# Kernel tuning notes

Measured on AMD Instinct MI355X. Metric: run time of the kernel, lower is better.

The kernel has to match this reference:

```python
import jax, jax.numpy as jnp
import numpy as np

N = 100000
E = 1600000
IN_DIM = 64
EMB_DIM = 64
BN_EPS = 1e-5


def setup_inputs() -> dict:
    key = jax.random.key(0)
    ks = jax.random.split(key, 8)
    x = jax.random.normal(ks[0], (N, IN_DIM), dtype=jnp.float32)
    edge_index = jax.random.randint(ks[1], (2, E), 0, N, dtype=jnp.int64)
    # GIN learned epsilon (train_eps=True), initialized to 0 as in PyG
    eps = jnp.zeros((), dtype=jnp.float32)
    # MLP params: Linear(in, emb) -> BN -> ReLU -> Linear(emb, emb)
    s1 = 1.0 / np.sqrt(IN_DIM)
    W1 = jax.random.uniform(ks[2], (IN_DIM, EMB_DIM), jnp.float32, -s1, s1)
    b1 = jax.random.uniform(ks[3], (EMB_DIM,), jnp.float32, -s1, s1)
    gamma = jnp.ones((EMB_DIM,), jnp.float32)
    beta = jnp.zeros((EMB_DIM,), jnp.float32)
    s2 = 1.0 / np.sqrt(EMB_DIM)
    W2 = jax.random.uniform(ks[4], (EMB_DIM, EMB_DIM), jnp.float32, -s2, s2)
    b2 = jax.random.uniform(ks[5], (EMB_DIM,), jnp.float32, -s2, s2)
    return {"x": x, "edge_index": edge_index, "eps": eps,
            "W1": W1, "b1": b1, "gamma": gamma, "beta": beta,
            "W2": W2, "b2": b2}


def reference(x, edge_index, eps, W1, b1, gamma, beta, W2, b2):
    src, dst = edge_index[0], edge_index[1]
    # GIN aggregation: sum of neighbor (source) features at each destination
    agg = jax.ops.segment_sum(x[src], dst, num_segments=N)  # [N, IN_DIM]
    h = (1.0 + eps) * x + agg
    # MLP: Linear -> BatchNorm1d (training-mode batch stats) -> ReLU -> Linear
    h1 = h @ W1 + b1                                   # [N, EMB_DIM]
    mean = jnp.mean(h1, axis=0)
    var = jnp.mean((h1 - mean) ** 2, axis=0)           # biased var, as torch BN
    h1n = (h1 - mean) * jax.lax.rsqrt(var + BN_EPS) * gamma + beta
    h2 = jax.nn.relu(h1n)
    return h2 @ W2 + b2                                # [N, EMB_DIM]
```

## Files before the change

kernel.cpp:

```cpp
#include <hip/hip_runtime.h>

#define NNODES 100000
#define NEDGES 1600000
#define DIM 64
#define NB 782
#define NPB 512
#define CHUNK 3125
#define CAP 3968
#define HP 72
#define NTILES 6250
#define NSLICE 32

typedef __attribute__((ext_vector_type(4))) float f32x4;
typedef __attribute__((ext_vector_type(8))) short s16x8;

__device__ __forceinline__ unsigned short bf16_rne(float f) {
  unsigned u = __float_as_uint(f);
  u += 0x7FFF + ((u >> 16) & 1);
  return (unsigned short)(u >> 16);
}
__device__ __forceinline__ float bf16_to_f32(unsigned short h) {
  return __uint_as_float(((unsigned)h) << 16);
}

__global__ __launch_bounds__(1024) void prep_part_kernel(
    const float* __restrict__ x, unsigned short* __restrict__ xb,
    const int* __restrict__ ei, int* __restrict__ gcursor,
    int* __restrict__ bpart,
    const float* __restrict__ W1, const float* __restrict__ W2,
    unsigned short* __restrict__ Wp1, unsigned short* __restrict__ Wp2) {
  __shared__ int sd[1024];
  __shared__ int delta[1024];
  __shared__ int lcur[1024];
  __shared__ int wsum[16];
  __shared__ int stage[CHUNK];
  __shared__ unsigned short sbuck[CHUNK + 1];
  int t = threadIdx.x;
  sd[t] = 0;
  for (int i = blockIdx.x * 1024 + t; i < NNODES * DIM / 4; i += NPB * 1024) {
    float4 v = ((const float4*)x)[i];
    ushort4 o;
    o.x = bf16_rne(v.x); o.y = bf16_rne(v.y);
    o.z = bf16_rne(v.z); o.w = bf16_rne(v.w);
    ((ushort4*)xb)[i] = o;
  }
  if (blockIdx.x == 0 && t < 128) {
    int lane = t & 63;
    const float* W = (t >= 64) ? W2 : W1;
    unsigned short* Wp = (t >= 64) ? Wp2 : Wp1;
    int q = lane >> 4, n16 = lane & 15;
#pragma unroll
    for (int f = 0; f < 8; ++f) {
      int kk = f >> 2, nt = f & 3;
#pragma unroll
      for (int j = 0; j < 8; ++j) {
        int k = kk * 32 + q * 8 + j;
        int n = nt * 16 + n16;
        Wp[f * 512 + lane * 8 + j] = bf16_rne(W[k * DIM + n]);
      }
    }
  }
  __syncthreads();
  int base = blockIdx.x * CHUNK;
  int es[4], ed[4];
#pragma unroll
  for (int j = 0; j < 4; ++j) {
    int i = t + j * 1024;
    bool ok = (i < CHUNK);
    es[j] = ok ? ei[base + i] : 0;
    ed[j] = ok ? ei[NEDGES + base + i] : -1;
    if (ok) atomicAdd(&sd[ed[j] >> 7], 1);
  }
  __syncthreads();
  int v = sd[t];
  int lane = t & 63;
  int incl = v;
#pragma unroll
  for (int off = 1; off < 64; off <<= 1) {
    int n = __shfl_up(incl, off);
    if (lane >= off) incl += n;
  }
  if (lane == 63) wsum[t >> 6] = incl;
  __syncthreads();
  if (t < 16) {
    int w = wsum[t];
#pragma unroll
    for (int off = 1; off < 16; off <<= 1) {
      int n = __shfl_up(w, off);
      if (t >= off) w += n;
    }
    wsum[t] = w;
  }
  __syncthreads();
  int wid = t >> 6;
  if (wid) incl += wsum[wid - 1];
  int excl = incl - v;
  delta[t] = (v ? (t * CAP + atomicAdd(&gcursor[t], v)) : 0) - excl;
  lcur[t] = excl;
  __syncthreads();
#pragma unroll
  for (int j = 0; j < 4; ++j) {
    int i = t + j * 1024;
    if (i < CHUNK) {
      int b = ed[j] >> 7;
      int p = atomicAdd(&lcur[b], 1);
      stage[p] = ((ed[j] & 127) << 17) | es[j];
      sbuck[p] = (unsigned short)b;
    }
  }
  __syncthreads();
  for (int i = t; i < CHUNK; i += 1024)
    bpart[delta[sbuck[i]] + i] = stage[i];
}

__global__ __launch_bounds__(512) void mega_kernel(
    const int* __restrict__ bpart, const int* __restrict__ gcursor,
    const unsigned short* __restrict__ xb, float* __restrict__ h1,
    const unsigned short* __restrict__ Wp, const float* __restrict__ b1,
    const float* __restrict__ epsp,
    float* __restrict__ sums32, float* __restrict__ sumsq32) {
  __shared__ int sd[128];
  __shared__ int cur[128];
  __shared__ int swv[4];
  __shared__ int stage[CAP];
  __shared__ __align__(16) unsigned short hbuf[128 * HP];
  __shared__ float lsum[DIM];
  __shared__ float lsq[DIM];
  int b = blockIdx.x;
  int t = threadIdx.x;
  if (t < 128) sd[t] = 0;
  if (t < DIM) { lsum[t] = 0.0f; lsq[t] = 0.0f; }
  __syncthreads();
  int pbase = b * CAP;
  int cnt = gcursor[b];
  int mv[8];
#pragma unroll
  for (int j = 0; j < 8; ++j) {
    int i = t + j * 512;
    mv[j] = (i < cnt) ? bpart[pbase + i] : -1;
    if (mv[j] >= 0) atomicAdd(&sd[mv[j] >> 17], 1);
  }
  __syncthreads();
  int deg = 0, incl = 0;
  if (t < 128) {
    deg = sd[t];
    incl = deg;
#pragma unroll
    for (int off = 1; off < 64; off <<= 1) {
      int n = __shfl_up(incl, off);
      if ((t & 63) >= off) incl += n;
    }
    if ((t & 63) == 63) swv[t >> 6] = incl;
  }
  __syncthreads();
  if (t < 128) {
    if (t >= 64) incl += swv[0];
    sd[t] = incl;
    cur[t] = incl - deg;
  }
  __syncthreads();
#pragma unroll
  for (int j = 0; j < 8; ++j) {
    if (mv[j] >= 0) {
      int p = atomicAdd(&cur[mv[j] >> 17], 1);
      stage[p] = mv[j] & 0x1FFFF;
    }
  }
  __syncthreads();
  {
    int part = t & 7;
    int half = (t >> 3) & 1;
    int ng = t >> 4;
#pragma unroll 1
    for (int pass = 0; pass < 4; ++pass) {
      int nl = ng + pass * 32;
      int e0 = (nl == 0) ? 0 : sd[nl - 1];
      int e1 = sd[nl];
      f32x4 aA0 = {0.f,0.f,0.f,0.f}, aA1 = aA0, aB0 = aA0, aB1 = aA0;
      int e = e0;
      for (; e + 8 <= e1; e += 8) {
        int s0 = stage[e + 0 + half];
        int s1 = stage[e + 2 + half];
        int s2 = stage[e + 4 + half];
        int s3 = stage[e + 6 + half];
        s16x8 u0 = *(const s16x8*)(xb + (size_t)s0 * DIM + part * 8);
        s16x8 u1 = *(const s16x8*)(xb + (size_t)s1 * DIM + part * 8);
        s16x8 u2 = *(const s16x8*)(xb + (size_t)s2 * DIM + part * 8);
        s16x8 u3 = *(const s16x8*)(xb + (size_t)s3 * DIM + part * 8);
#pragma unroll
        for (int j = 0; j < 4; ++j) {
          aA0[j] += bf16_to_f32((unsigned short)u0[j]) +
                    bf16_to_f32((unsigned short)u2[j]);
          aA1[j] += bf16_to_f32((unsigned short)u0[j + 4]) +
                    bf16_to_f32((unsigned short)u2[j + 4]);
          aB0[j] += bf16_to_f32((unsigned short)u1[j]) +
                    bf16_to_f32((unsigned short)u3[j]);
          aB1[j] += bf16_to_f32((unsigned short)u1[j + 4]) +
                    bf16_to_f32((unsigned short)u3[j + 4]);
        }
      }
      for (; e + 2 <= e1; e += 2) {
        int s = stage[e + half];
        s16x8 u = *(const s16x8*)(xb + (size_t)s * DIM + part * 8);
#pragma unroll
        for (int j = 0; j < 4; ++j) {
          aA0[j] += bf16_to_f32((unsigned short)u[j]);
          aA1[j] += bf16_to_f32((unsigned short)u[j + 4]);
        }
      }
      if (e < e1 && half == 0) {
        int s = stage[e];
        s16x8 u = *(const s16x8*)(xb + (size_t)s * DIM + part * 8);
#pragma unroll
        for (int j = 0; j < 4; ++j) {
          aA0[j] += bf16_to_f32((unsigned short)u[j]);
          aA1[j] += bf16_to_f32((unsigned short)u[j + 4]);
        }
      }
      float r[8];
#pragma unroll
      for (int j = 0; j < 4; ++j) {
        r[j] = aA0[j] + aB0[j];
        r[j + 4] = aA1[j] + aB1[j];
      }
      s16x8 o;
#pragma unroll
      for (int j = 0; j < 8; ++j)
        o[j] = (short)bf16_rne(r[j] + __shfl_down(r[j], 8));
      if (half == 0)
        *(s16x8*)&hbuf[nl * HP + part * 8] = o;
    }
  }
  __syncthreads();
  {
    int wave = t >> 6;
    int lane = t & 63;
    int tile = b * 8 + wave;
    if (tile < NTILES) {
      int q = lane >> 4;
      int r16 = lane & 15;
      float onep = 1.0f + epsp[0];
      int lrow = wave * 16 + r16;
      int grow = b * 128 + lrow;
      const s16x8* xrow = (const s16x8*)(xb + (size_t)grow * DIM);
      f32x4 acc[4] = {{0.f,0.f,0.f,0.f},{0.f,0.f,0.f,0.f},
                      {0.f,0.f,0.f,0.f},{0.f,0.f,0.f,0.f}};
#pragma unroll
      for (int kk = 0; kk < 2; ++kk) {
        s16x8 xv = xrow[kk * 4 + q];
        s16x8 hv = *(const s16x8*)&hbuf[lrow * HP + kk * 32 + q * 8];
        s16x8 a;
#pragma unroll
        for (int j = 0; j < 8; ++j)
          a[j] = (short)bf16_rne(fmaf(onep,
                     bf16_to_f32((unsigned short)xv[j]),
                     bf16_to_f32((unsigned short)hv[j])));
#pragma unroll
        for (int nt = 0; nt < 4; ++nt) {
          s16x8 bfk = ((const s16x8*)Wp)[(kk * 4 + nt) * 64 + lane];
          acc[nt] = __builtin_amdgcn_mfma_f32_16x16x32_bf16(
              a, bfk, acc[nt], 0, 0, 0);
        }
      }
      int orow = tile * 16 + q * 4;
#pragma unroll
      for (int nt = 0; nt < 4; ++nt) {
        int col = nt * 16 + r16;
        float bb = b1[col];
        float sl = 0.0f, ql = 0.0f;
#pragma unroll
        for (int r = 0; r < 4; ++r) {
          float v = acc[nt][r] + bb;
          h1[(size_t)(orow + r) * DIM + col] = v;
          sl += v;
          ql = fmaf(v, v, ql);
        }
        sl += __shfl_down(sl, 32); ql += __shfl_down(ql, 32);
        sl += __shfl_down(sl, 16); ql += __shfl_down(ql, 16);
        if (q == 0) {
          atomicAdd(&lsum[col], sl);
          atomicAdd(&lsq[col], ql);
        }
      }
    }
  }
  __syncthreads();
  if (t < DIM) {
    int sl = (b & (NSLICE - 1)) * DIM;
    atomicAdd(&sums32[sl + t], lsum[t]);
    atomicAdd(&sumsq32[sl + t], lsq[t]);
  }
}

__global__ __launch_bounds__(256) void fused2_kernel(
    const float* __restrict__ h1, float* __restrict__ out,
    const unsigned short* __restrict__ Wp, const float* __restrict__ b2,
    const float* __restrict__ gamma, const float* __restrict__ beta,
    const float* __restrict__ sums32, const float* __restrict__ sumsq32) {
  __shared__ float sc_s[DIM];
  __shared__ float sh_s[DIM];
  int t = threadIdx.x;
  if (t < DIM) {
    float s = 0.0f, q2 = 0.0f;
#pragma unroll
    for (int j = 0; j < NSLICE; ++j) {
      s  += sums32[j * DIM + t];
      q2 += sumsq32[j * DIM + t];
    }
    float invN = 1.0f / (float)NNODES;
    float m = s * invN;
    float v = fmaf(-m, m, q2 * invN);
    float sc = gamma[t] * rsqrtf(v + 1e-5f);
    sc_s[t] = sc;
    sh_s[t] = fmaf(-m, sc, beta[t]);
  }
  __syncthreads();
  int wave = t >> 6;
  int lane = t & 63;
  int tile = blockIdx.x * 4 + wave;
  if (tile >= NTILES) return;
  int q = lane >> 4;
  int r16 = lane & 15;
  s16x8 bf[8];
#pragma unroll
  for (int f = 0; f < 8; ++f)
    bf[f] = ((const s16x8*)Wp)[f * 64 + lane];
  int arow = tile * 16 + r16;
  const float* hr = h1 + (size_t)arow * DIM + q * 8;
  f32x4 acc[4] = {{0.f,0.f,0.f,0.f},{0.f,0.f,0.f,0.f},
                  {0.f,0.f,0.f,0.f},{0.f,0.f,0.f,0.f}};
#pragma unroll
  for (int kk = 0; kk < 2; ++kk) {
    int kbase = kk * 32 + q * 8;
    float4 hv0 = *(const float4*)(hr + kk * 32);
    float4 hv1 = *(const float4*)(hr + kk * 32 + 4);
    float4 sc0 = *(const float4*)(sc_s + kbase);
    float4 sc1 = *(const float4*)(sc_s + kbase + 4);
    float4 sh0 = *(const float4*)(sh_s + kbase);
    float4 sh1 = *(const float4*)(sh_s + kbase + 4);
    s16x8 a;
    a[0] = (short)bf16_rne(fmaxf(fmaf(hv0.x, sc0.x, sh0.x), 0.f));
    a[1] = (short)bf16_rne(fmaxf(fmaf(hv0.y, sc0.y, sh0.y), 0.f));
    a[2] = (short)bf16_rne(fmaxf(fmaf(hv0.z, sc0.z, sh0.z), 0.f));
    a[3] = (short)bf16_rne(fmaxf(fmaf(hv0.w, sc0.w, sh0.w), 0.f));
    a[4] = (short)bf16_rne(fmaxf(fmaf(hv1.x, sc1.x, sh1.x), 0.f));
    a[5] = (short)bf16_rne(fmaxf(fmaf(hv1.y, sc1.y, sh1.y), 0.f));
    a[6] = (short)bf16_rne(fmaxf(fmaf(hv1.z, sc1.z, sh1.z), 0.f));
    a[7] = (short)bf16_rne(fmaxf(fmaf(hv1.w, sc1.w, sh1.w), 0.f));
#pragma unroll
    for (int nt = 0; nt < 4; ++nt)
      acc[nt] = __builtin_amdgcn_mfma_f32_16x16x32_bf16(
          a, bf[kk * 4 + nt], acc[nt], 0, 0, 0);
  }
  int orow = tile * 16 + q * 4;
#pragma unroll
  for (int nt = 0; nt < 4; ++nt) {
    int col = nt * 16 + r16;
    float bb = b2[col];
#pragma unroll
    for (int r = 0; r < 4; ++r)
      out[(size_t)(orow + r) * DIM + col] = acc[nt][r] + bb;
  }
}

extern "C" void kernel_launch(void* const* d_in, const int* in_sizes, int n_in,
                              void* d_out, int out_size, void* d_ws, size_t ws_size,
                              hipStream_t stream) {
  (void)in_sizes; (void)n_in; (void)out_size; (void)ws_size;
  const float* x     = (const float*)d_in[0];
  const int*   ei    = (const int*)d_in[1];
  const float* eps   = (const float*)d_in[2];
  const float* W1    = (const float*)d_in[3];
  const float* b1    = (const float*)d_in[4];
  const float* gamma = (const float*)d_in[5];
  const float* beta  = (const float*)d_in[6];
  const float* W2    = (const float*)d_in[7];
  const float* b2    = (const float*)d_in[8];
  float* outp = (float*)d_out;

  const int N = NNODES;

  float* h1       = (float*)d_ws;
  float* sums32   = h1 + (size_t)N * DIM;
  float* sumsq32  = sums32 + NSLICE * DIM;
  int*   gcursor  = (int*)(sumsq32 + NSLICE * DIM);
  unsigned short* Wp1 = (unsigned short*)(gcursor + 1024);
  unsigned short* Wp2 = Wp1 + 4096;
  int*            bpart = (int*)d_out;
  unsigned short* xb    = (unsigned short*)d_out + (size_t)NB * CAP * 2;

  hipMemsetAsync(sums32, 0,
                 (size_t)(2 * NSLICE * DIM) * sizeof(float) + 1024 * sizeof(int),
                 stream);
  prep_part_kernel<<<NPB, 1024, 0, stream>>>(x, xb, ei, gcursor, bpart,
                                             W1, W2, Wp1, Wp2);
  mega_kernel     <<<NB, 512, 0, stream>>>(bpart, gcursor, xb, h1,
                                           Wp1, b1, eps, sums32, sumsq32);
  fused2_kernel   <<<(NTILES + 3) / 4, 256, 0, stream>>>(h1, outp, Wp2, b2,
                                                         gamma, beta,
                                                         sums32, sumsq32);
}
```

Baseline: 162.3 us.

## Halve destination bucket size to 64 nodes and fold self-term into aggregation

```diff
diff --git a/kernel.cpp b/kernel.cpp
--- a/kernel.cpp
+++ b/kernel.cpp
@@ -3,10 +3,11 @@
 #define NNODES 100000
 #define NEDGES 1600000
 #define DIM 64
-#define NB 782
+#define NB 1563
+#define NBP 1568
 #define NPB 512
 #define CHUNK 3125
-#define CAP 3968
+#define CAP 2032
 #define HP 72
 #define NTILES 6250
 #define NSLICE 32
@@ -29,14 +30,14 @@
     int* __restrict__ bpart,
     const float* __restrict__ W1, const float* __restrict__ W2,
     unsigned short* __restrict__ Wp1, unsigned short* __restrict__ Wp2) {
-  __shared__ int sd[1024];
-  __shared__ int delta[1024];
-  __shared__ int lcur[1024];
+  __shared__ int sd[NBP];
+  __shared__ int delta[NBP];
+  __shared__ int lcur[NBP];
   __shared__ int wsum[16];
   __shared__ int stage[CHUNK];
   __shared__ unsigned short sbuck[CHUNK + 1];
   int t = threadIdx.x;
-  sd[t] = 0;
+  for (int i = t; i < NBP; i += 1024) sd[i] = 0;
   for (int i = blockIdx.x * 1024 + t; i < NNODES * DIM / 4; i += NPB * 1024) {
     float4 v = ((const float4*)x)[i];
     ushort4 o;
@@ -69,12 +70,14 @@
     bool ok = (i < CHUNK);
     es[j] = ok ? ei[base + i] : 0;
     ed[j] = ok ? ei[NEDGES + base + i] : -1;
-    if (ok) atomicAdd(&sd[ed[j] >> 7], 1);
-  }
-  __syncthreads();
-  int v = sd[t];
+    if (ok) atomicAdd(&sd[ed[j] >> 6], 1);
+  }
+  __syncthreads();
+  int e0 = 0, e1 = 0;
+  if (t < 782) { e0 = sd[2 * t]; e1 = sd[2 * t + 1]; }
+  int p = e0 + e1;
   int lane = t & 63;
-  int incl = v;
+  int incl = p;
 #pragma unroll
   for (int off = 1; off < 64; off <<= 1) {
     int n = __shfl_up(incl, off);
@@ -94,18 +97,24 @@
   __syncthreads();
   int wid = t >> 6;
   if (wid) incl += wsum[wid - 1];
-  int excl = incl - v;
-  delta[t] = (v ? (t * CAP + atomicAdd(&gcursor[t], v)) : 0) - excl;
-  lcur[t] = excl;
+  if (t < 782) {
+    int s0 = incl - p;
+    int s1 = s0 + e0;
+    int b0 = 2 * t, b1 = 2 * t + 1;
+    delta[b0] = (e0 ? (b0 * CAP + atomicAdd(&gcursor[b0], e0)) : 0) - s0;
+    delta[b1] = (e1 ? (b1 * CAP + atomicAdd(&gcursor[b1], e1)) : 0) - s1;
+    lcur[b0] = s0;
+    lcur[b1] = s1;
+  }
   __syncthreads();
 #pragma unroll
   for (int j = 0; j < 4; ++j) {
     int i = t + j * 1024;
     if (i < CHUNK) {
-      int b = ed[j] >> 7;
-      int p = atomicAdd(&lcur[b], 1);
-      stage[p] = ((ed[j] & 127) << 17) | es[j];
-      sbuck[p] = (unsigned short)b;
+      int b = ed[j] >> 6;
+      int pp = atomicAdd(&lcur[b], 1);
+      stage[pp] = ((ed[j] & 63) << 17) | es[j];
+      sbuck[pp] = (unsigned short)b;
     }
   }
   __syncthreads();
@@ -113,48 +122,40 @@
     bpart[delta[sbuck[i]] + i] = stage[i];
 }
 
-__global__ __launch_bounds__(512) void mega_kernel(
+__global__ __launch_bounds__(256, 8) void mega_kernel(
     const int* __restrict__ bpart, const int* __restrict__ gcursor,
     const unsigned short* __restrict__ xb, float* __restrict__ h1,
     const unsigned short* __restrict__ Wp, const float* __restrict__ b1,
     const float* __restrict__ epsp,
     float* __restrict__ sums32, float* __restrict__ sumsq32) {
-  __shared__ int sd[128];
-  __shared__ int cur[128];
-  __shared__ int swv[4];
+  __shared__ int sd[64];
+  __shared__ int cur[64];
   __shared__ int stage[CAP];
-  __shared__ __align__(16) unsigned short hbuf[128 * HP];
+  __shared__ __align__(16) unsigned short hbuf[64 * HP];
   __shared__ float lsum[DIM];
   __shared__ float lsq[DIM];
   int b = blockIdx.x;
   int t = threadIdx.x;
-  if (t < 128) sd[t] = 0;
-  if (t < DIM) { lsum[t] = 0.0f; lsq[t] = 0.0f; }
+  if (t < 64) { sd[t] = 0; lsum[t] = 0.0f; lsq[t] = 0.0f; }
   __syncthreads();
   int pbase = b * CAP;
   int cnt = gcursor[b];
   int mv[8];
 #pragma unroll
   for (int j = 0; j < 8; ++j) {
-    int i = t + j * 512;
+    int i = t + j * 256;
     mv[j] = (i < cnt) ? bpart[pbase + i] : -1;
     if (mv[j] >= 0) atomicAdd(&sd[mv[j] >> 17], 1);
   }
   __syncthreads();
-  int deg = 0, incl = 0;
-  if (t < 128) {
-    deg = sd[t];
-    incl = deg;
+  if (t < 64) {
+    int deg = sd[t];
+    int incl = deg;
 #pragma unroll
     for (int off = 1; off < 64; off <<= 1) {
       int n = __shfl_up(incl, off);
-      if ((t & 63) >= off) incl += n;
-    }
-    if ((t & 63) == 63) swv[t >> 6] = incl;
-  }
-  __syncthreads();
-  if (t < 128) {
-    if (t >= 64) incl += swv[0];
+      if (t >= off) incl += n;
+    }
     sd[t] = incl;
     cur[t] = incl - deg;
   }
@@ -171,11 +172,15 @@
     int part = t & 7;
     int half = (t >> 3) & 1;
     int ng = t >> 4;
+    float onep = 1.0f + epsp[0];
 #pragma unroll 1
     for (int pass = 0; pass < 4; ++pass) {
-      int nl = ng + pass * 32;
+      int nl = ng + pass * 16;
       int e0 = (nl == 0) ? 0 : sd[nl - 1];
       int e1 = sd[nl];
+      s16x8 xpre = {0, 0, 0, 0, 0, 0, 0, 0};
+      if (half == 0)
+        xpre = *(const s16x8*)(xb + (size_t)(b * 64 + nl) * DIM + part * 8);
       f32x4 aA0 = {0.f,0.f,0.f,0.f}, aA1 = aA0, aB0 = aA0, aB1 = aA0;
       int e = e0;
       for (; e + 8 <= e1; e += 8) {
@@ -225,8 +230,11 @@
       }
       s16x8 o;
 #pragma unroll
-      for (int j = 0; j < 8; ++j)
-        o[j] = (short)bf16_rne(r[j] + __shfl_down(r[j], 8));
+      for (int j = 0; j < 8; ++j) {
+        float s2 = r[j] + __shfl_down(r[j], 8);
+        o[j] = (short)bf16_rne(fmaf(onep,
+                   bf16_to_f32((unsigned short)xpre[j]), s2));
+      }
       if (half == 0)
         *(s16x8*)&hbuf[nl * HP + part * 8] = o;
     }
@@ -235,26 +243,16 @@
   {
     int wave = t >> 6;
     int lane = t & 63;
-    int tile = b * 8 + wave;
+    int tile = b * 4 + wave;
     if (tile < NTILES) {
       int q = lane >> 4;
       int r16 = lane & 15;
-      float onep = 1.0f + epsp[0];
       int lrow = wave * 16 + r16;
-      int grow = b * 128 + lrow;
-      const s16x8* xrow = (const s16x8*)(xb + (size_t)grow * DIM);
       f32x4 acc[4] = {{0.f,0.f,0.f,0.f},{0.f,0.f,0.f,0.f},
                       {0.f,0.f,0.f,0.f},{0.f,0.f,0.f,0.f}};
 #pragma unroll
       for (int kk = 0; kk < 2; ++kk) {
-        s16x8 xv = xrow[kk * 4 + q];
-        s16x8 hv = *(const s16x8*)&hbuf[lrow * HP + kk * 32 + q * 8];
-        s16x8 a;
-#pragma unroll
-        for (int j = 0; j < 8; ++j)
-          a[j] = (short)bf16_rne(fmaf(onep,
-                     bf16_to_f32((unsigned short)xv[j]),
-                     bf16_to_f32((unsigned short)hv[j])));
+        s16x8 a = *(const s16x8*)&hbuf[lrow * HP + kk * 32 + q * 8];
 #pragma unroll
         for (int nt = 0; nt < 4; ++nt) {
           s16x8 bfk = ((const s16x8*)Wp)[(kk * 4 + nt) * 64 + lane];
@@ -384,17 +382,17 @@
   float* sums32   = h1 + (size_t)N * DIM;
   float* sumsq32  = sums32 + NSLICE * DIM;
   int*   gcursor  = (int*)(sumsq32 + NSLICE * DIM);
-  unsigned short* Wp1 = (unsigned short*)(gcursor + 1024);
+  unsigned short* Wp1 = (unsigned short*)(gcursor + NBP);
   unsigned short* Wp2 = Wp1 + 4096;
   int*            bpart = (int*)d_out;
   unsigned short* xb    = (unsigned short*)d_out + (size_t)NB * CAP * 2;
 
   hipMemsetAsync(sums32, 0,
-                 (size_t)(2 * NSLICE * DIM) * sizeof(float) + 1024 * sizeof(int),
+                 (size_t)(2 * NSLICE * DIM) * sizeof(float) + NBP * sizeof(int),
                  stream);
   prep_part_kernel<<<NPB, 1024, 0, stream>>>(x, xb, ei, gcursor, bpart,
                                              W1, W2, Wp1, Wp2);
-  mega_kernel     <<<NB, 512, 0, stream>>>(bpart, gcursor, xb, h1,
+  mega_kernel     <<<NB, 256, 0, stream>>>(bpart, gcursor, xb, h1,
                                            Wp1, b1, eps, sums32, sumsq32);
   fused2_kernel   <<<(NTILES + 3) / 4, 256, 0, stream>>>(h1, outp, Wp2, b2,
                                                          gamma, beta,
```

Result: slower. 189.4 us (+16.7%).
